# Kernel optimization log

Hardware: AMD Instinct MI355X
Metric: run time of the kernel (lower is better)

## Reference

```python
import jax, jax.numpy as jnp
import numpy as np

# GLIFR constants (defaults from GLIFS_ASC / GLIFR paper)
DT = 0.05
DELAY = int(1.0 / DT)   # synaptic delay in steps = 20
SIGMA_V = 1.0           # sigmoid smoothing of spiking
V_RESET = 0.0
R_MEM = 0.1             # membrane resistance
I0 = 0.0                # baseline current

B, T, I, H, O, A = 64, 200, 512, 2048, 512, 2


def setup_inputs() -> dict:
    key = jax.random.key(0)
    ks = jax.random.split(key, 8)
    return {
        "x": jax.random.normal(ks[0], (B, T, I), jnp.float32),
        "weight_iv": jax.random.normal(ks[1], (I, H), jnp.float32) / np.sqrt(I),
        "weight_lat": jax.random.normal(ks[2], (H, H), jnp.float32) / np.sqrt(H),
        "thresh": 1.0 + 0.1 * jax.random.normal(ks[3], (1, H), jnp.float32),
        "k_m": jnp.full((1, H), 0.05, jnp.float32),              # membrane rate 1/tau
        "asc_amp": 0.01 * jax.random.normal(ks[4], (A, 1, H), jnp.float32),  # additive ASC jump a_k
        "asc_r": 0.01 * jax.random.normal(ks[5], (A, 1, H), jnp.float32),    # multiplicative ASC reset r_k
        "asc_k": jnp.ones((A, 1, H), jnp.float32),               # ASC decay rate k_k
        "w_out": jax.random.normal(ks[6], (H, O), jnp.float32) / np.sqrt(H),
        "b_out": jnp.zeros((O,), jnp.float32),
    }


def glifr_forward(x, weight_iv, weight_lat, thresh, k_m, asc_amp, asc_r, asc_k, w_out, b_out):
    # Precompute the feed-forward synaptic drive for all steps at once: (B,T,H)
    syn_in = jnp.einsum("bti,ih->bth", x, weight_iv)
    asc_decay = jnp.exp(-DT * asc_k)  # (A,1,H)

    firing0 = jnp.zeros((B, H), x.dtype)
    volt0 = jnp.zeros((B, H), x.dtype)
    asc0 = jnp.zeros((A, B, H), x.dtype)
    buf0 = jnp.zeros((DELAY, B, H), x.dtype)  # delay line of past firing rates

    def step(carry, syn_t):
        firing, voltage, ascur, buf = carry
        delayed = buf[0]  # firing from DELAY steps ago (zeros initially)
        syncurrent = syn_t + delayed @ weight_lat  # (B,H)
        # after-spike currents: exponential decay + smoothed spike-triggered update
        ascur = ascur * asc_decay + firing[None] * (asc_r * ascur + asc_amp)
        total_in = syncurrent + ascur.sum(0) + I0
        # smoothed voltage reset, then Euler leak/integration
        voltage = voltage * (1.0 - firing) + V_RESET * firing
        voltage = voltage + DT * k_m * (R_MEM * total_in - voltage)
        # smoothed firing (sigmoid of normalized voltage above threshold)
        firing = jax.nn.sigmoid((voltage - thresh) / SIGMA_V)
        buf = jnp.concatenate([buf[1:], firing[None]], axis=0)
        return (firing, voltage, ascur, buf), firing

    _, firing_seq = jax.lax.scan(step, (firing0, volt0, asc0, buf0), jnp.swapaxes(syn_in, 0, 1))
    firing_seq = jnp.swapaxes(firing_seq, 0, 1)  # (B,T,H)
    # dropout_prob=0 and silence_mult=I are identities; output Linear applied per step
    return jnp.einsum("bth,ho->bto", firing_seq, w_out) + b_out


def reference(x, weight_iv, weight_lat, thresh, k_m, asc_amp, asc_r, asc_k, w_out, b_out):
    return glifr_forward(x, weight_iv, weight_lat, thresh, k_m, asc_amp, asc_r, asc_k, w_out, b_out)
```

## Files before the change

### kernel.cpp

```cpp
#include <hip/hip_runtime.h>
#include <hip/hip_bf16.h>


#define B_ 64
#define T_ 200
#define I_ 512
#define H_ 2048
#define O_ 512
#define BH_ 131072
#define DELAY_ 20
#define DT_ 0.05f
#define RMEM_ 0.1f

typedef __bf16 bf16x8 __attribute__((ext_vector_type(8)));
typedef float f32x4 __attribute__((ext_vector_type(4)));

__device__ __forceinline__ unsigned short f2bf(float f) {
    unsigned int u = __builtin_bit_cast(unsigned int, f);
    u = (u + 0x7fff + ((u >> 16) & 1)) >> 16;
    return (unsigned short)u;
}
__device__ __forceinline__ float bf2f(unsigned short u) {
    return __builtin_bit_cast(float, (unsigned int)u << 16);
}

__device__ __forceinline__ void gload16(const void* g, void* l) {
    __builtin_amdgcn_global_load_lds(
        (const __attribute__((address_space(1))) unsigned int*)g,
        (__attribute__((address_space(3))) unsigned int*)l, 16, 0, 0);
}

__global__ void k_cvt_tb(const float* __restrict__ in, unsigned short* __restrict__ out) {
    int g = blockIdx.x * 256 + threadIdx.x;
    int idx = g * 4;
    int r = idx >> 9;
    int i0 = idx & 511;
    int t = r >> 6, b = r & 63;
    float4 v = *(const float4*)(in + ((size_t)b * T_ + t) * I_ + i0);
    ushort4 o;
    o.x = f2bf(v.x); o.y = f2bf(v.y); o.z = f2bf(v.z); o.w = f2bf(v.w);
    *(ushort4*)(out + idx) = o;
}

__global__ __launch_bounds__(256) void k_tcvt(const float* __restrict__ in,
                                              unsigned short* __restrict__ out,
                                              int R, int C, int ldo, int ooff) {
    __shared__ float t[32][33];
    int bx = blockIdx.x, by = blockIdx.y;
    int tx = threadIdx.x & 31, ty = threadIdx.x >> 5;
    #pragma unroll
    for (int r = 0; r < 32; r += 8)
        t[ty + r][tx] = in[(size_t)(by * 32 + ty + r) * C + bx * 32 + tx];
    __syncthreads();
    #pragma unroll
    for (int r = 0; r < 32; r += 8)
        out[(size_t)(bx * 32 + ty + r) * ldo + ooff + by * 32 + tx] = f2bf(t[tx][ty + r]);
}

template<int BM, int BN, int WGM, int WGN>
__global__ __launch_bounds__(WGM * WGN * 64) void k_gemm(
    const unsigned short* __restrict__ A1, const unsigned short* __restrict__ A2,
    const unsigned short* __restrict__ Bt, void* __restrict__ Cv,
    const float* __restrict__ bias,
    int k1, int K, int lda1, int lda2, int ldbt, int kboff, int ldc,
    int cmap, int cbf16, int ksplit, long long csplit, int gx, int gy)
{
    constexpr int NT = WGM * WGN * 64;
    constexpr int AIT = (BM * 8) / NT, BIT = (BN * 8) / NT;
    constexpr int ASZ = BM * 64, BSZ = BN * 64;
    constexpr int WTM = BM / WGM, WTN = BN / WGN;
    constexpr int FM = WTM / 16, FN = WTN / 16;
    constexpr int SMAIN = 2 * (ASZ + BSZ) * 2;
    constexpr int SEPI = BM * BN * 4;
    constexpr int SBYTES = SMAIN > SEPI ? SMAIN : SEPI;
    __shared__ char smem[SBYTES];
    unsigned short* As = (unsigned short*)smem;
    unsigned short* Bs = As + 2 * ASZ;

    const int nb = gx * gy * ksplit;
    const int hw = blockIdx.x;
    const int wid = (hw & 7) * (nb >> 3) + (hw >> 3);
    const int layer = gx * gy;
    const int split = wid / layer;
    const int w2 = wid % layer;
    int bm, bn;
    if (gx <= gy) { bn = w2 % gx; bm = w2 / gx; }
    else          { bm = w2 % gy; bn = w2 / gy; }

    const int klen = K / ksplit;
    const int nk = klen >> 6;
    const int kb = (split * klen) >> 6;

    const int tid = threadIdx.x;
    const int lane = tid & 63, wave = tid >> 6;
    const int wr = (wave / WGN) * WTM, wc = (wave % WGN) * WTN;
    const int fr = lane & 15, kg = lane >> 4;
    const int rx = fr & 7;

    int arow[AIT], acg[AIT], lsA[AIT];
    #pragma unroll
    for (int it = 0; it < AIT; ++it) {
        int s = tid + it * NT;
        int row = s >> 3, cp = s & 7;
        acg[it] = (cp ^ (row & 7)) * 8;
        arow[it] = bm * BM + row;
        lsA[it] = s * 8;
    }
    const unsigned short* Bp[BIT]; int lsB[BIT];
    #pragma unroll
    for (int it = 0; it < BIT; ++it) {
        int s = tid + it * NT;
        int row = s >> 3, cp = s & 7, cg = cp ^ (row & 7);
        Bp[it] = Bt + (size_t)(bn * BN + row) * ldbt + kboff + cg * 8;
        lsB[it] = s * 8;
    }

    auto stage = [&](int buf, int ktg) {
        const int kc = ktg << 6;
        #pragma unroll
        for (int it = 0; it < AIT; ++it) {
            int kcol = kc + acg[it];
            const unsigned short* p = (kcol < k1)
                ? A1 + (size_t)arow[it] * lda1 + kcol
                : A2 + (size_t)arow[it] * lda2 + (kcol - k1);
            gload16(p, &As[buf * ASZ + lsA[it]]);
        }
        #pragma unroll
        for (int it = 0; it < BIT; ++it)
            gload16(Bp[it] + kc, &Bs[buf * BSZ + lsB[it]]);
    };

    f32x4 acc[FM][FN] = {};

    stage(0, kb);
    __syncthreads();
    for (int t = 0; t < nk; ++t) {
        const int cur = t & 1;
        if (t + 1 < nk) stage(cur ^ 1, kb + t + 1);
        #pragma unroll
        for (int kk = 0; kk < 2; ++kk) {
            const int ck = (kk << 2) | kg;
            bf16x8 af[FM], bfr[FN];
            #pragma unroll
            for (int i = 0; i < FM; ++i)
                af[i] = *(const bf16x8*)(&As[cur * ASZ + (wr + i * 16 + fr) * 64 + ((ck ^ rx) << 3)]);
            #pragma unroll
            for (int j = 0; j < FN; ++j)
                bfr[j] = *(const bf16x8*)(&Bs[cur * BSZ + (wc + j * 16 + fr) * 64 + ((ck ^ rx) << 3)]);
            #pragma unroll
            for (int i = 0; i < FM; ++i)
                #pragma unroll
                for (int j = 0; j < FN; ++j)
                    acc[i][j] = __builtin_amdgcn_mfma_f32_16x16x32_bf16(af[i], bfr[j], acc[i][j], 0, 0, 0);
        }
        __syncthreads();
    }

    if (cbf16) {
        unsigned short* Cs = (unsigned short*)smem;
        #pragma unroll
        for (int i = 0; i < FM; ++i)
            #pragma unroll
            for (int j = 0; j < FN; ++j)
                #pragma unroll
                for (int r = 0; r < 4; ++r)
                    Cs[(wr + i * 16 + kg * 4 + r) * BN + wc + j * 16 + fr] = f2bf(acc[i][j][r]);
        __syncthreads();
        unsigned short* Cb = (unsigned short*)Cv + (size_t)split * csplit;
        constexpr int NCH = BM * BN / 8;
        #pragma unroll
        for (int s0 = 0; s0 < NCH; s0 += NT) {
            int s = s0 + tid;
            if (NCH % NT != 0 && s >= NCH) break;
            int row = s / (BN / 8), c8 = s % (BN / 8);
            int m = bm * BM + row;
            *(uint4*)(Cb + (size_t)m * ldc + bn * BN + c8 * 8) = *(const uint4*)&Cs[row * BN + c8 * 8];
        }
    } else {
        float* Cs = (float*)smem;
        #pragma unroll
        for (int i = 0; i < FM; ++i)
            #pragma unroll
            for (int j = 0; j < FN; ++j) {
                int col = bn * BN + wc + j * 16 + fr;
                float b = bias ? bias[col] : 0.f;
                #pragma unroll
                for (int r = 0; r < 4; ++r)
                    Cs[(wr + i * 16 + kg * 4 + r) * BN + wc + j * 16 + fr] = acc[i][j][r] + b;
            }
        __syncthreads();
        float* Cf = (float*)Cv;
        constexpr int NCH = BM * BN / 4;
        #pragma unroll
        for (int s0 = 0; s0 < NCH; s0 += NT) {
            int s = s0 + tid;
            if (NCH % NT != 0 && s >= NCH) break;
            int row = s / (BN / 4), c4 = s % (BN / 4);
            int m = bm * BM + row;
            int cr = cmap ? ((m & 63) * 200 + (m >> 6)) : m;
            *(float4*)(Cf + (size_t)cr * ldc + bn * BN + c4 * 4) = *(const float4*)&Cs[row * BN + c4 * 4];
        }
    }
}

template<int NP>
__global__ __launch_bounds__(128) void k_rec(
    const unsigned short* __restrict__ P, unsigned short* __restrict__ F,
    float* __restrict__ volt, float* __restrict__ fire, float* __restrict__ asc,
    const float* __restrict__ thresh, const float* __restrict__ km,
    const float* __restrict__ asc_amp, const float* __restrict__ asc_r,
    const float* __restrict__ asc_k, int t0)
{
    const size_t PSPL = (size_t)DELAY_ * BH_;
    int base = (blockIdx.x * 128 + threadIdx.x) * 4;
    int h = base & (H_ - 1);
    float v[4], f[4], a0[4], a1[4], th[4], dtk[4], amp0[4], amp1[4], r0[4], r1[4], d0[4], d1[4];
    *(float4*)v  = *(const float4*)(volt + base);
    *(float4*)f  = *(const float4*)(fire + base);
    *(float4*)a0 = *(const float4*)(asc + base);
    *(float4*)a1 = *(const float4*)(asc + BH_ + base);
    *(float4*)th = *(const float4*)(thresh + h);
    *(float4*)amp0 = *(const float4*)(asc_amp + h);
    *(float4*)amp1 = *(const float4*)(asc_amp + H_ + h);
    *(float4*)r0 = *(const float4*)(asc_r + h);
    *(float4*)r1 = *(const float4*)(asc_r + H_ + h);
    #pragma unroll
    for (int q = 0; q < 4; ++q) {
        dtk[q] = DT_ * km[h + q];
        d0[q] = expf(-DT_ * asc_k[h + q]);
        d1[q] = expf(-DT_ * asc_k[H_ + h + q]);
    }
    ushort4 pa[NP], pb[NP];
    #pragma unroll
    for (int s = 0; s < NP; ++s) pa[s] = *(const ushort4*)(P + s * PSPL + base);
    for (int t = 0; t < DELAY_; ++t) {
        if (t + 1 < DELAY_) {
            #pragma unroll
            for (int s = 0; s < NP; ++s)
                pb[s] = *(const ushort4*)(P + s * PSPL + (size_t)(t + 1) * BH_ + base);
        }
        ushort4 o4;
        unsigned short* op = (unsigned short*)&o4;
        #pragma unroll
        for (int q = 0; q < 4; ++q) {
            float syn = 0.f;
            #pragma unroll
            for (int s = 0; s < NP; ++s) syn += bf2f(((const unsigned short*)&pa[s])[q]);
            float na0 = a0[q] * d0[q] + f[q] * (r0[q] * a0[q] + amp0[q]);
            float na1 = a1[q] * d1[q] + f[q] * (r1[q] * a1[q] + amp1[q]);
            a0[q] = na0; a1[q] = na1;
            float tot = syn + a0[q] + a1[q];
            v[q] = v[q] * (1.f - f[q]);
            v[q] = v[q] + dtk[q] * (RMEM_ * tot - v[q]);
            f[q] = 1.f / (1.f + __expf(-(v[q] - th[q])));
            op[q] = f2bf(f[q]);
        }
        *(ushort4*)(F + (size_t)(t0 + t) * BH_ + base) = o4;
        #pragma unroll
        for (int s = 0; s < NP; ++s) pa[s] = pb[s];
    }
    *(float4*)(volt + base) = *(float4*)v;
    *(float4*)(fire + base) = *(float4*)f;
    *(float4*)(asc + base) = *(float4*)a0;
    *(float4*)(asc + BH_ + base) = *(float4*)a1;
}

extern "C" void kernel_launch(void* const* d_in, const int* in_sizes, int n_in,
                              void* d_out, int out_size, void* d_ws, size_t ws_size,
                              hipStream_t stream) {
    const float* x       = (const float*)d_in[0];
    const float* w_iv    = (const float*)d_in[1];
    const float* w_lat   = (const float*)d_in[2];
    const float* thresh  = (const float*)d_in[3];
    const float* km      = (const float*)d_in[4];
    const float* asc_amp = (const float*)d_in[5];
    const float* asc_r   = (const float*)d_in[6];
    const float* asc_k   = (const float*)d_in[7];
    const float* w_out   = (const float*)d_in[8];
    const float* b_out   = (const float*)d_in[9];
    float* out = (float*)d_out;

    char* ws = (char*)d_ws;
    unsigned short* P     = (unsigned short*)ws;
    unsigned short* Fb    = (unsigned short*)(ws + 10485760);
    unsigned short* xbt   = (unsigned short*)(ws + 62914560);
    unsigned short* WcatT = (unsigned short*)(ws + 76021760);
    unsigned short* WoutT = (unsigned short*)(ws + 86507520);
    float*          volt  = (float*)(ws + 88604672);
    float*          fire  = (float*)(ws + 89128960);
    float*          asc   = (float*)(ws + 89653248);

    k_cvt_tb<<<(T_ * B_ * I_ / 4) / 256, 256, 0, stream>>>(x, xbt);
    k_tcvt<<<dim3(H_ / 32, H_ / 32), 256, 0, stream>>>(w_lat, WcatT, H_, H_, 2560, 0);
    k_tcvt<<<dim3(H_ / 32, I_ / 32), 256, 0, stream>>>(w_iv, WcatT, I_, H_, 2560, 2048);
    k_tcvt<<<dim3(O_ / 32, H_ / 32), 256, 0, stream>>>(w_out, WoutT, H_, O_, 2048, 0);
    hipMemsetAsync(volt, 0, 524288 + 524288 + 1048576, stream);

    k_gemm<64, 64, 4, 2><<<(DELAY_ * B_ / 64) * (H_ / 64), 512, 0, stream>>>(
        nullptr, xbt, WcatT, P, nullptr,
        0, I_, 0, I_, 2560, 2048, H_, 0, 1, 1, 0, H_ / 64, DELAY_ * B_ / 64);
    k_rec<1><<<256, 128, 0, stream>>>(P, Fb, volt, fire, asc,
                                      thresh, km, asc_amp, asc_r, asc_k, 0);

    for (int c = 1; c < T_ / DELAY_; ++c) {
        k_gemm<128, 64, 4, 2><<<(DELAY_ * B_ / 128) * (H_ / 64) * 2, 512, 0, stream>>>(
            Fb + (size_t)(c - 1) * DELAY_ * BH_, xbt + (size_t)c * DELAY_ * B_ * I_,
            WcatT, P, nullptr,
            H_, H_ + I_, H_, I_, 2560, 0, H_, 0, 1, 2, (long long)DELAY_ * BH_,
            H_ / 64, DELAY_ * B_ / 128);
        k_rec<2><<<256, 128, 0, stream>>>(P, Fb, volt, fire, asc,
                                          thresh, km, asc_amp, asc_r, asc_k, c * DELAY_);
    }

    k_gemm<128, 128, 4, 4><<<(B_ * T_ / 128) * (O_ / 128), 1024, 0, stream>>>(
        nullptr, Fb, WoutT, out, b_out,
        0, H_, 0, H_, H_, 0, O_, 1, 0, 1, 0, O_ / 128, B_ * T_ / 128);
}
```

Before: 351.1 us.

## Fuse per-chunk output projection into recurrent lateral GEMM launches

The GEMM kernel now takes two job descriptors and splits its grid between them. Each chunk launch computes the lateral/input drive for chunk c and also the output projection for the already-finished chunk c-1. This replaces the one large final output GEMM with 80 extra blocks added to each of the nine recurrent launches plus a small tail launch. The aim is to fill idle GPU slots during the latency-bound recurrence and shorten the serial tail, at the cost of a smaller 128x64 tile for the output GEMM and some runtime job selection overhead.

Result: slower. 384.9 us (+9.6%).

```diff
diff --git a/kernel.cpp b/kernel.cpp
--- a/kernel.cpp
+++ b/kernel.cpp
@@ -57,14 +57,20 @@
         out[(size_t)(bx * 32 + ty + r) * ldo + ooff + by * 32 + tx] = f2bf(t[tx][ty + r]);
 }
 
+struct GJob {
+    const unsigned short* A1;
+    const unsigned short* A2;
+    const unsigned short* Bt;
+    void* Cv;
+    const float* bias;
+    int k1, K, lda1, lda2, ldbt, kboff, ldc;
+    int cmap, coff, cbf16, ksplit;
+    long long csplit;
+    int gx, gy;
+};
+
 template<int BM, int BN, int WGM, int WGN>
-__global__ __launch_bounds__(WGM * WGN * 64) void k_gemm(
-    const unsigned short* __restrict__ A1, const unsigned short* __restrict__ A2,
-    const unsigned short* __restrict__ Bt, void* __restrict__ Cv,
-    const float* __restrict__ bias,
-    int k1, int K, int lda1, int lda2, int ldbt, int kboff, int ldc,
-    int cmap, int cbf16, int ksplit, long long csplit, int gx, int gy)
-{
+__global__ __launch_bounds__(WGM * WGN * 64) void k_gemm(GJob j0, GJob j1, int n0) {
     constexpr int NT = WGM * WGN * 64;
     constexpr int AIT = (BM * 8) / NT, BIT = (BN * 8) / NT;
     constexpr int ASZ = BM * 64, BSZ = BN * 64;
@@ -77,17 +83,19 @@
     unsigned short* As = (unsigned short*)smem;
     unsigned short* Bs = As + 2 * ASZ;
 
-    const int nb = gx * gy * ksplit;
     const int hw = blockIdx.x;
-    const int wid = (hw & 7) * (nb >> 3) + (hw >> 3);
-    const int layer = gx * gy;
+    const GJob J = (hw < n0) ? j0 : j1;
+    const int lb = (hw < n0) ? hw : hw - n0;
+    const int nb = J.gx * J.gy * J.ksplit;
+    const int wid = (lb & 7) * (nb >> 3) + (lb >> 3);
+    const int layer = J.gx * J.gy;
     const int split = wid / layer;
     const int w2 = wid % layer;
     int bm, bn;
-    if (gx <= gy) { bn = w2 % gx; bm = w2 / gx; }
-    else          { bm = w2 % gy; bn = w2 / gy; }
-
-    const int klen = K / ksplit;
+    if (J.gx <= J.gy) { bn = w2 % J.gx; bm = w2 / J.gx; }
+    else              { bm = w2 % J.gy; bn = w2 / J.gy; }
+
+    const int klen = J.K / J.ksplit;
     const int nk = klen >> 6;
     const int kb = (split * klen) >> 6;
 
@@ -111,7 +119,7 @@
     for (int it = 0; it < BIT; ++it) {
         int s = tid + it * NT;
         int row = s >> 3, cp = s & 7, cg = cp ^ (row & 7);
-        Bp[it] = Bt + (size_t)(bn * BN + row) * ldbt + kboff + cg * 8;
+        Bp[it] = J.Bt + (size_t)(bn * BN + row) * J.ldbt + J.kboff + cg * 8;
         lsB[it] = s * 8;
     }
 
@@ -120,9 +128,9 @@
         #pragma unroll
         for (int it = 0; it < AIT; ++it) {
             int kcol = kc + acg[it];
-            const unsigned short* p = (kcol < k1)
-                ? A1 + (size_t)arow[it] * lda1 + kcol
-                : A2 + (size_t)arow[it] * lda2 + (kcol - k1);
+            const unsigned short* p = (kcol < J.k1)
+                ? J.A1 + (size_t)arow[it] * J.lda1 + kcol
+                : J.A2 + (size_t)arow[it] * J.lda2 + (kcol - J.k1);
             gload16(p, &As[buf * ASZ + lsA[it]]);
         }
         #pragma unroll
@@ -156,7 +164,7 @@
         __syncthreads();
     }
 
-    if (cbf16) {
+    if (J.cbf16) {
         unsigned short* Cs = (unsigned short*)smem;
         #pragma unroll
         for (int i = 0; i < FM; ++i)
@@ -166,7 +174,7 @@
                 for (int r = 0; r < 4; ++r)
                     Cs[(wr + i * 16 + kg * 4 + r) * BN + wc + j * 16 + fr] = f2bf(acc[i][j][r]);
         __syncthreads();
-        unsigned short* Cb = (unsigned short*)Cv + (size_t)split * csplit;
+        unsigned short* Cb = (unsigned short*)J.Cv + (size_t)split * J.csplit;
         constexpr int NCH = BM * BN / 8;
         #pragma unroll
         for (int s0 = 0; s0 < NCH; s0 += NT) {
@@ -174,7 +182,7 @@
             if (NCH % NT != 0 && s >= NCH) break;
             int row = s / (BN / 8), c8 = s % (BN / 8);
             int m = bm * BM + row;
-            *(uint4*)(Cb + (size_t)m * ldc + bn * BN + c8 * 8) = *(const uint4*)&Cs[row * BN + c8 * 8];
+            *(uint4*)(Cb + (size_t)m * J.ldc + bn * BN + c8 * 8) = *(const uint4*)&Cs[row * BN + c8 * 8];
         }
     } else {
         float* Cs = (float*)smem;
@@ -183,13 +191,13 @@
             #pragma unroll
             for (int j = 0; j < FN; ++j) {
                 int col = bn * BN + wc + j * 16 + fr;
-                float b = bias ? bias[col] : 0.f;
+                float b = J.bias ? J.bias[col] : 0.f;
                 #pragma unroll
                 for (int r = 0; r < 4; ++r)
                     Cs[(wr + i * 16 + kg * 4 + r) * BN + wc + j * 16 + fr] = acc[i][j][r] + b;
             }
         __syncthreads();
-        float* Cf = (float*)Cv;
+        float* Cf = (float*)J.Cv;
         constexpr int NCH = BM * BN / 4;
         #pragma unroll
         for (int s0 = 0; s0 < NCH; s0 += NT) {
@@ -197,8 +205,8 @@
             if (NCH % NT != 0 && s >= NCH) break;
             int row = s / (BN / 4), c4 = s % (BN / 4);
             int m = bm * BM + row;
-            int cr = cmap ? ((m & 63) * 200 + (m >> 6)) : m;
-            *(float4*)(Cf + (size_t)cr * ldc + bn * BN + c4 * 4) = *(const float4*)&Cs[row * BN + c4 * 4];
+            int cr = J.cmap ? ((m & 63) * 200 + (m >> 6) + J.coff) : m;
+            *(float4*)(Cf + (size_t)cr * J.ldc + bn * BN + c4 * 4) = *(const float4*)&Cs[row * BN + c4 * 4];
         }
     }
 }
@@ -296,23 +304,55 @@
     k_tcvt<<<dim3(O_ / 32, H_ / 32), 256, 0, stream>>>(w_out, WoutT, H_, O_, 2048, 0);
     hipMemsetAsync(volt, 0, 524288 + 524288 + 1048576, stream);
 
-    k_gemm<64, 64, 4, 2><<<(DELAY_ * B_ / 64) * (H_ / 64), 512, 0, stream>>>(
-        nullptr, xbt, WcatT, P, nullptr,
-        0, I_, 0, I_, 2560, 2048, H_, 0, 1, 1, 0, H_ / 64, DELAY_ * B_ / 64);
+    auto latJob = [&](int c) {
+        GJob j;
+        j.A1 = Fb + (size_t)(c - 1) * DELAY_ * BH_;
+        j.A2 = xbt + (size_t)c * DELAY_ * B_ * I_;
+        j.Bt = WcatT; j.Cv = P; j.bias = nullptr;
+        j.k1 = H_; j.K = H_ + I_; j.lda1 = H_; j.lda2 = I_;
+        j.ldbt = 2560; j.kboff = 0; j.ldc = H_;
+        j.cmap = 0; j.coff = 0; j.cbf16 = 1; j.ksplit = 2;
+        j.csplit = (long long)DELAY_ * BH_;
+        j.gx = H_ / 64; j.gy = DELAY_ * B_ / 128;
+        return j;
+    };
+    auto outJob = [&](int c) {
+        GJob j;
+        j.A1 = Fb + (size_t)c * DELAY_ * BH_;
+        j.A2 = j.A1; j.Bt = WoutT; j.Cv = out; j.bias = b_out;
+        j.k1 = H_; j.K = H_; j.lda1 = H_; j.lda2 = H_;
+        j.ldbt = H_; j.kboff = 0; j.ldc = O_;
+        j.cmap = 1; j.coff = c * DELAY_; j.cbf16 = 0; j.ksplit = 1;
+        j.csplit = 0;
+        j.gx = O_ / 64; j.gy = DELAY_ * B_ / 128;
+        return j;
+    };
+    auto c0Job = [&]() {
+        GJob j;
+        j.A1 = xbt; j.A2 = xbt; j.Bt = WcatT; j.Cv = P; j.bias = nullptr;
+        j.k1 = 0; j.K = I_; j.lda1 = I_; j.lda2 = I_;
+        j.ldbt = 2560; j.kboff = 2048; j.ldc = H_;
+        j.cmap = 0; j.coff = 0; j.cbf16 = 1; j.ksplit = 1;
+        j.csplit = 0;
+        j.gx = H_ / 64; j.gy = DELAY_ * B_ / 64;
+        return j;
+    };
+
+    {
+        GJob j = c0Job();
+        k_gemm<64, 64, 4, 2><<<640, 512, 0, stream>>>(j, j, 640);
+    }
     k_rec<1><<<256, 128, 0, stream>>>(P, Fb, volt, fire, asc,
                                       thresh, km, asc_amp, asc_r, asc_k, 0);
 
     for (int c = 1; c < T_ / DELAY_; ++c) {
-        k_gemm<128, 64, 4, 2><<<(DELAY_ * B_ / 128) * (H_ / 64) * 2, 512, 0, stream>>>(
-            Fb + (size_t)(c - 1) * DELAY_ * BH_, xbt + (size_t)c * DELAY_ * B_ * I_,
-            WcatT, P, nullptr,
-            H_, H_ + I_, H_, I_, 2560, 0, H_, 0, 1, 2, (long long)DELAY_ * BH_,
-            H_ / 64, DELAY_ * B_ / 128);
+        k_gemm<128, 64, 4, 2><<<720, 512, 0, stream>>>(outJob(c - 1), latJob(c), 80);
         k_rec<2><<<256, 128, 0, stream>>>(P, Fb, volt, fire, asc,
                                           thresh, km, asc_amp, asc_r, asc_k, c * DELAY_);
     }
 
-    k_gemm<128, 128, 4, 4><<<(B_ * T_ / 128) * (O_ / 128), 1024, 0, stream>>>(
-        nullptr, Fb, WoutT, out, b_out,
-        0, H_, 0, H_, H_, 0, O_, 1, 0, 1, 0, O_ / 128, B_ * T_ / 128);
-}
+    {
+        GJob j = outJob(9);
+        k_gemm<128, 64, 4, 2><<<80, 512, 0, stream>>>(j, j, 80);
+    }
+}
```

## Use FP8 operands for input and recurrent GEMMs in the scan

Applied to the files above, without the earlier changes.

Converts x, weight_iv and weight_lat to FP8 and runs the per-chunk input and lateral GEMMs with fp8 MFMA at a 128-wide K tile. The recurrence kernel now also writes an FP8 copy of the firing rates for the next chunk's GEMM, while the output GEMM stays in bf16. The goal is to halve operand bytes and double MFMA throughput on the serial GEMM path. The cost is much coarser precision, with no scaling, on the recurrent weights and the sigmoid outputs, which may break the accuracy tolerance, plus an extra FP8 store per step.

Result: no change. 354.1 us (+0.9%).

```diff
diff --git a/kernel.cpp b/kernel.cpp
--- a/kernel.cpp
+++ b/kernel.cpp
@@ -23,6 +23,10 @@
 __device__ __forceinline__ float bf2f(unsigned short u) {
     return __builtin_bit_cast(float, (unsigned int)u << 16);
 }
+__device__ __forceinline__ unsigned int pk4fp8(float a, float b, float c, float d) {
+    unsigned int lo = __builtin_amdgcn_cvt_pk_fp8_f32(a, b, 0, 0);
+    return __builtin_amdgcn_cvt_pk_fp8_f32(c, d, lo, 1);
+}
 
 __device__ __forceinline__ void gload16(const void* g, void* l) {
     __builtin_amdgcn_global_load_lds(
@@ -30,16 +34,14 @@
         (__attribute__((address_space(3))) unsigned int*)l, 16, 0, 0);
 }
 
-__global__ void k_cvt_tb(const float* __restrict__ in, unsigned short* __restrict__ out) {
+__global__ void k_cvt_tb(const float* __restrict__ in, unsigned char* __restrict__ out) {
     int g = blockIdx.x * 256 + threadIdx.x;
     int idx = g * 4;
     int r = idx >> 9;
     int i0 = idx & 511;
     int t = r >> 6, b = r & 63;
     float4 v = *(const float4*)(in + ((size_t)b * T_ + t) * I_ + i0);
-    ushort4 o;
-    o.x = f2bf(v.x); o.y = f2bf(v.y); o.z = f2bf(v.z); o.w = f2bf(v.w);
-    *(ushort4*)(out + idx) = o;
+    *(unsigned int*)(out + idx) = pk4fp8(v.x, v.y, v.z, v.w);
 }
 
 __global__ __launch_bounds__(256) void k_tcvt(const float* __restrict__ in,
@@ -57,25 +59,47 @@
         out[(size_t)(bx * 32 + ty + r) * ldo + ooff + by * 32 + tx] = f2bf(t[tx][ty + r]);
 }
 
-template<int BM, int BN, int WGM, int WGN>
+__global__ __launch_bounds__(256) void k_tcvt8(const float* __restrict__ in,
+                                               unsigned char* __restrict__ out,
+                                               int R, int C, int ldo, int ooff) {
+    __shared__ float t[32][33];
+    int bx = blockIdx.x, by = blockIdx.y;
+    int tx = threadIdx.x & 31, ty = threadIdx.x >> 5;
+    #pragma unroll
+    for (int r = 0; r < 32; r += 8)
+        t[ty + r][tx] = in[(size_t)(by * 32 + ty + r) * C + bx * 32 + tx];
+    __syncthreads();
+    #pragma unroll
+    for (int r = 0; r < 32; r += 8) {
+        unsigned int p = __builtin_amdgcn_cvt_pk_fp8_f32(t[tx][ty + r], 0.f, 0, 0);
+        out[(size_t)(bx * 32 + ty + r) * ldo + ooff + by * 32 + tx] = (unsigned char)(p & 0xFF);
+    }
+}
+
+template<int BM, int BN, int WGM, int WGN, int EFP8>
 __global__ __launch_bounds__(WGM * WGN * 64) void k_gemm(
-    const unsigned short* __restrict__ A1, const unsigned short* __restrict__ A2,
-    const unsigned short* __restrict__ Bt, void* __restrict__ Cv,
-    const float* __restrict__ bias,
+    const void* A1v, const void* A2v, const void* Btv, void* Cv,
+    const float* bias,
     int k1, int K, int lda1, int lda2, int ldbt, int kboff, int ldc,
     int cmap, int cbf16, int ksplit, long long csplit, int gx, int gy)
 {
+    constexpr int ES = EFP8 ? 1 : 2;
+    constexpr int KT = EFP8 ? 128 : 64;
     constexpr int NT = WGM * WGN * 64;
+    constexpr int ASZ = BM * 128, BSZ = BN * 128;
     constexpr int AIT = (BM * 8) / NT, BIT = (BN * 8) / NT;
-    constexpr int ASZ = BM * 64, BSZ = BN * 64;
     constexpr int WTM = BM / WGM, WTN = BN / WGN;
     constexpr int FM = WTM / 16, FN = WTN / 16;
-    constexpr int SMAIN = 2 * (ASZ + BSZ) * 2;
+    constexpr int SMAIN = 2 * (ASZ + BSZ);
     constexpr int SEPI = BM * BN * 4;
     constexpr int SBYTES = SMAIN > SEPI ? SMAIN : SEPI;
     __shared__ char smem[SBYTES];
-    unsigned short* As = (unsigned short*)smem;
-    unsigned short* Bs = As + 2 * ASZ;
+    char* As = smem;
+    char* Bs = smem + 2 * ASZ;
+
+    const char* A1 = (const char*)A1v;
+    const char* A2 = (const char*)A2v;
+    const char* Bt = (const char*)Btv;
 
     const int nb = gx * gy * ksplit;
     const int hw = blockIdx.x;
@@ -88,8 +112,8 @@
     else          { bm = w2 % gy; bn = w2 / gy; }
 
     const int klen = K / ksplit;
-    const int nk = klen >> 6;
-    const int kb = (split * klen) >> 6;
+    const int nk = klen / KT;
+    const int kb = (split * klen) / KT;
 
     const int tid = threadIdx.x;
     const int lane = tid & 63, wave = tid >> 6;
@@ -97,37 +121,37 @@
     const int fr = lane & 15, kg = lane >> 4;
     const int rx = fr & 7;
 
-    int arow[AIT], acg[AIT], lsA[AIT];
+    int arow[AIT], acgE[AIT], lsA[AIT];
     #pragma unroll
     for (int it = 0; it < AIT; ++it) {
         int s = tid + it * NT;
         int row = s >> 3, cp = s & 7;
-        acg[it] = (cp ^ (row & 7)) * 8;
+        acgE[it] = (cp ^ (row & 7)) * (16 / ES);
         arow[it] = bm * BM + row;
-        lsA[it] = s * 8;
-    }
-    const unsigned short* Bp[BIT]; int lsB[BIT];
+        lsA[it] = s * 16;
+    }
+    const char* Bp[BIT]; int lsB[BIT];
     #pragma unroll
     for (int it = 0; it < BIT; ++it) {
         int s = tid + it * NT;
-        int row = s >> 3, cp = s & 7, cg = cp ^ (row & 7);
-        Bp[it] = Bt + (size_t)(bn * BN + row) * ldbt + kboff + cg * 8;
-        lsB[it] = s * 8;
+        int row = s >> 3, cp = s & 7;
+        Bp[it] = Bt + ((size_t)(bn * BN + row) * ldbt + kboff + (cp ^ (row & 7)) * (16 / ES)) * ES;
+        lsB[it] = s * 16;
     }
 
     auto stage = [&](int buf, int ktg) {
-        const int kc = ktg << 6;
+        const int kc = ktg * KT;
         #pragma unroll
         for (int it = 0; it < AIT; ++it) {
-            int kcol = kc + acg[it];
-            const unsigned short* p = (kcol < k1)
-                ? A1 + (size_t)arow[it] * lda1 + kcol
-                : A2 + (size_t)arow[it] * lda2 + (kcol - k1);
+            int kcol = kc + acgE[it];
+            const char* p = (kcol < k1)
+                ? A1 + ((size_t)arow[it] * lda1 + kcol) * ES
+                : A2 + ((size_t)arow[it] * lda2 + (kcol - k1)) * ES;
             gload16(p, &As[buf * ASZ + lsA[it]]);
         }
         #pragma unroll
         for (int it = 0; it < BIT; ++it)
-            gload16(Bp[it] + kc, &Bs[buf * BSZ + lsB[it]]);
+            gload16(Bp[it] + (size_t)kc * ES, &Bs[buf * BSZ + lsB[it]]);
     };
 
     f32x4 acc[FM][FN] = {};
@@ -137,21 +161,40 @@
     for (int t = 0; t < nk; ++t) {
         const int cur = t & 1;
         if (t + 1 < nk) stage(cur ^ 1, kb + t + 1);
-        #pragma unroll
-        for (int kk = 0; kk < 2; ++kk) {
-            const int ck = (kk << 2) | kg;
-            bf16x8 af[FM], bfr[FN];
-            #pragma unroll
-            for (int i = 0; i < FM; ++i)
-                af[i] = *(const bf16x8*)(&As[cur * ASZ + (wr + i * 16 + fr) * 64 + ((ck ^ rx) << 3)]);
-            #pragma unroll
-            for (int j = 0; j < FN; ++j)
-                bfr[j] = *(const bf16x8*)(&Bs[cur * BSZ + (wc + j * 16 + fr) * 64 + ((ck ^ rx) << 3)]);
-            #pragma unroll
-            for (int i = 0; i < FM; ++i)
+        if constexpr (EFP8) {
+            #pragma unroll
+            for (int kk = 0; kk < 4; ++kk) {
+                const int cb = (((2 * kk + (kg >> 1)) ^ rx) << 4) + ((kg & 1) << 3);
+                long af[FM], bfr[FN];
+                #pragma unroll
+                for (int i = 0; i < FM; ++i)
+                    af[i] = *(const long*)(&As[cur * ASZ + (wr + i * 16 + fr) * 128 + cb]);
                 #pragma unroll
                 for (int j = 0; j < FN; ++j)
-                    acc[i][j] = __builtin_amdgcn_mfma_f32_16x16x32_bf16(af[i], bfr[j], acc[i][j], 0, 0, 0);
+                    bfr[j] = *(const long*)(&Bs[cur * BSZ + (wc + j * 16 + fr) * 128 + cb]);
+                #pragma unroll
+                for (int i = 0; i < FM; ++i)
+                    #pragma unroll
+                    for (int j = 0; j < FN; ++j)
+                        acc[i][j] = __builtin_amdgcn_mfma_f32_16x16x32_fp8_fp8(af[i], bfr[j], acc[i][j], 0, 0, 0);
+            }
+        } else {
+            #pragma unroll
+            for (int kk = 0; kk < 2; ++kk) {
+                const int ck = (kk << 2) | kg;
+                bf16x8 af[FM], bfr[FN];
+                #pragma unroll
+                for (int i = 0; i < FM; ++i)
+                    af[i] = *(const bf16x8*)(&As[cur * ASZ + (wr + i * 16 + fr) * 128 + ((ck ^ rx) << 4)]);
+                #pragma unroll
+                for (int j = 0; j < FN; ++j)
+                    bfr[j] = *(const bf16x8*)(&Bs[cur * BSZ + (wc + j * 16 + fr) * 128 + ((ck ^ rx) << 4)]);
+                #pragma unroll
+                for (int i = 0; i < FM; ++i)
+                    #pragma unroll
+                    for (int j = 0; j < FN; ++j)
+                        acc[i][j] = __builtin_amdgcn_mfma_f32_16x16x32_bf16(af[i], bfr[j], acc[i][j], 0, 0, 0);
+            }
         }
         __syncthreads();
     }
@@ -206,6 +249,7 @@
 template<int NP>
 __global__ __launch_bounds__(128) void k_rec(
     const unsigned short* __restrict__ P, unsigned short* __restrict__ F,
+    unsigned char* __restrict__ F8,
     float* __restrict__ volt, float* __restrict__ fire, float* __restrict__ asc,
     const float* __restrict__ thresh, const float* __restrict__ km,
     const float* __restrict__ asc_amp, const float* __restrict__ asc_r,
@@ -256,6 +300,7 @@
             op[q] = f2bf(f[q]);
         }
         *(ushort4*)(F + (size_t)(t0 + t) * BH_ + base) = o4;
+        *(unsigned int*)(F8 + (size_t)(t0 + t) * BH_ + base) = pk4fp8(f[0], f[1], f[2], f[3]);
         #pragma unroll
         for (int s = 0; s < NP; ++s) pa[s] = pb[s];
     }
@@ -282,37 +327,38 @@
 
     char* ws = (char*)d_ws;
     unsigned short* P     = (unsigned short*)ws;
-    unsigned short* Fb    = (unsigned short*)(ws + 10485760);
-    unsigned short* xbt   = (unsigned short*)(ws + 62914560);
-    unsigned short* WcatT = (unsigned short*)(ws + 76021760);
-    unsigned short* WoutT = (unsigned short*)(ws + 86507520);
-    float*          volt  = (float*)(ws + 88604672);
-    float*          fire  = (float*)(ws + 89128960);
-    float*          asc   = (float*)(ws + 89653248);
-
-    k_cvt_tb<<<(T_ * B_ * I_ / 4) / 256, 256, 0, stream>>>(x, xbt);
-    k_tcvt<<<dim3(H_ / 32, H_ / 32), 256, 0, stream>>>(w_lat, WcatT, H_, H_, 2560, 0);
-    k_tcvt<<<dim3(H_ / 32, I_ / 32), 256, 0, stream>>>(w_iv, WcatT, I_, H_, 2560, 2048);
+    unsigned short* F16   = (unsigned short*)(ws + 10485760);
+    unsigned char*  F8    = (unsigned char*)(ws + 62914560);
+    unsigned char*  xbt8  = (unsigned char*)(ws + 89128960);
+    unsigned char*  Wcat8 = (unsigned char*)(ws + 95682560);
+    unsigned short* WoutT = (unsigned short*)(ws + 100925440);
+    float*          volt  = (float*)(ws + 103022592);
+    float*          fire  = (float*)(ws + 103546880);
+    float*          asc   = (float*)(ws + 104071168);
+
+    k_cvt_tb<<<(T_ * B_ * I_ / 4) / 256, 256, 0, stream>>>(x, xbt8);
+    k_tcvt8<<<dim3(H_ / 32, H_ / 32), 256, 0, stream>>>(w_lat, Wcat8, H_, H_, 2560, 0);
+    k_tcvt8<<<dim3(H_ / 32, I_ / 32), 256, 0, stream>>>(w_iv, Wcat8, I_, H_, 2560, 2048);
     k_tcvt<<<dim3(O_ / 32, H_ / 32), 256, 0, stream>>>(w_out, WoutT, H_, O_, 2048, 0);
     hipMemsetAsync(volt, 0, 524288 + 524288 + 1048576, stream);
 
-    k_gemm<64, 64, 4, 2><<<(DELAY_ * B_ / 64) * (H_ / 64), 512, 0, stream>>>(
-        nullptr, xbt, WcatT, P, nullptr,
-        0, I_, 0, I_, 2560, 2048, H_, 0, 1, 1, 0, H_ / 64, DELAY_ * B_ / 64);
-    k_rec<1><<<256, 128, 0, stream>>>(P, Fb, volt, fire, asc,
+    k_gemm<64, 64, 4, 2, 1><<<(DELAY_ * B_ / 64) * (H_ / 64), 512, 0, stream>>>(
+        nullptr, xbt8, Wcat8, P, nullptr,
+        0, I_, I_, I_, 2560, 2048, H_, 0, 1, 1, 0, H_ / 64, DELAY_ * B_ / 64);
+    k_rec<1><<<256, 128, 0, stream>>>(P, F16, F8, volt, fire, asc,
                                       thresh, km, asc_amp, asc_r, asc_k, 0);
 
     for (int c = 1; c < T_ / DELAY_; ++c) {
-        k_gemm<128, 64, 4, 2><<<(DELAY_ * B_ / 128) * (H_ / 64) * 2, 512, 0, stream>>>(
-            Fb + (size_t)(c - 1) * DELAY_ * BH_, xbt + (size_t)c * DELAY_ * B_ * I_,
-            WcatT, P, nullptr,
+        k_gemm<128, 64, 4, 2, 1><<<(DELAY_ * B_ / 128) * (H_ / 64) * 2, 512, 0, stream>>>(
+            F8 + (size_t)(c - 1) * DELAY_ * BH_, xbt8 + (size_t)c * DELAY_ * B_ * I_,
+            Wcat8, P, nullptr,
             H_, H_ + I_, H_, I_, 2560, 0, H_, 0, 1, 2, (long long)DELAY_ * BH_,
             H_ / 64, DELAY_ * B_ / 128);
-        k_rec<2><<<256, 128, 0, stream>>>(P, Fb, volt, fire, asc,
+        k_rec<2><<<256, 128, 0, stream>>>(P, F16, F8, volt, fire, asc,
                                           thresh, km, asc_amp, asc_r, asc_k, c * DELAY_);
     }
 
-    k_gemm<128, 128, 4, 4><<<(B_ * T_ / 128) * (O_ / 128), 1024, 0, stream>>>(
-        nullptr, Fb, WoutT, out, b_out,
-        0, H_, 0, H_, H_, 0, O_, 1, 0, 1, 0, O_ / 128, B_ * T_ / 128);
-}
+    k_gemm<128, 128, 4, 4, 0><<<(B_ * T_ / 128) * (O_ / 128), 1024, 0, stream>>>(
+        nullptr, F16, WoutT, out, b_out,
+        0, H_, H_, H_, H_, 0, O_, 1, 0, 1, 0, O_ / 128, B_ * T_ / 128);
+}
```
